# Kernel optimization log

Hardware: AMD Instinct MI355X
Metric: run time of the kernel (lower is better)

The kernel has to match this reference:

```python
import jax, jax.numpy as jnp
import numpy as np

TEMP = 0.07


def setup_inputs() -> dict:
    key = jax.random.key(0)
    k1, k2 = jax.random.split(key)
    N, C = 8192, 512
    X = jax.random.normal(k1, (N, C), dtype=jnp.float32)
    Y = jax.random.normal(k2, (N, C), dtype=jnp.float32)
    return {"X": X, "Y": Y}


def reference(X, Y):
    # Original loop computes, per row i, cross-entropy over logits
    # [X_i.Y_i, X_i.Y_j (j != i)] / temp with label 0 (the positive).
    # Softmax CE is permutation-invariant, so this equals
    #   logsumexp(S_i / temp) - S_ii / temp,  S = X @ Y^T,
    # summed over rows (loop accumulates with +=, i.e. sum reduction).
    S = jnp.einsum('nc,mc->nm', X, Y) / TEMP  # [N, N]
    lse = jax.nn.logsumexp(S, axis=1)          # [N]
    pos = jnp.diagonal(S)                      # [N]
    return jnp.sum(lse - pos)
```

## Files before the change

kernel.cpp:

```cpp
#include <hip/hip_runtime.h>
#include <stdint.h>

#define N 8192
#define C 512
#define BM 128
#define BN 128
#define BKF 128
#define NSPLIT 8
#define COLS_PER_SPLIT (N / NSPLIT)
#define CT (COLS_PER_SPLIT / BN)
#define GRID_GEMM (64 * NSPLIT)
#define INV_T 14.285714285714286f

typedef __attribute__((ext_vector_type(4)))  int   i32x4;
typedef __attribute__((ext_vector_type(8)))  int   i32x8;
typedef __attribute__((ext_vector_type(16))) float f32x16;

__global__ __launch_bounds__(256) void prep_kernel(const float* __restrict__ X,
                                                   const float* __restrict__ Y,
                                                   unsigned char* __restrict__ Xf8,
                                                   unsigned char* __restrict__ Yf8,
                                                   float* __restrict__ pos) {
  const int wave = threadIdx.x >> 6;
  const int lane = threadIdx.x & 63;
  const int row = blockIdx.x * 4 + wave;
  const float4* xr = (const float4*)(X + (size_t)row * C) + lane * 2;
  const float4* yr = (const float4*)(Y + (size_t)row * C) + lane * 2;
  float4 x0 = xr[0], x1 = xr[1];
  float4 y0 = yr[0], y1 = yr[1];
  float s = x0.x * y0.x + x0.y * y0.y + x0.z * y0.z + x0.w * y0.w
          + x1.x * y1.x + x1.y * y1.y + x1.z * y1.z + x1.w * y1.w;
  int2 ox, oy;
  ox.x = __builtin_amdgcn_cvt_pk_fp8_f32(x0.x, x0.y, 0, false);
  ox.x = __builtin_amdgcn_cvt_pk_fp8_f32(x0.z, x0.w, ox.x, true);
  ox.y = __builtin_amdgcn_cvt_pk_fp8_f32(x1.x, x1.y, 0, false);
  ox.y = __builtin_amdgcn_cvt_pk_fp8_f32(x1.z, x1.w, ox.y, true);
  oy.x = __builtin_amdgcn_cvt_pk_fp8_f32(y0.x, y0.y, 0, false);
  oy.x = __builtin_amdgcn_cvt_pk_fp8_f32(y0.z, y0.w, oy.x, true);
  oy.y = __builtin_amdgcn_cvt_pk_fp8_f32(y1.x, y1.y, 0, false);
  oy.y = __builtin_amdgcn_cvt_pk_fp8_f32(y1.z, y1.w, oy.y, true);
  ((int2*)(Xf8 + (size_t)row * C))[lane] = ox;
  ((int2*)(Yf8 + (size_t)row * C))[lane] = oy;
#pragma unroll
  for (int off = 32; off >= 1; off >>= 1) s += __shfl_xor(s, off);
  if (lane == 0) pos[row] = s * INV_T;
}

__global__ __launch_bounds__(256, 2) void gemm_lse_kernel(const unsigned char* __restrict__ Xf8,
                                                          const unsigned char* __restrict__ Yf8,
                                                          float2* __restrict__ partials) {
  __shared__ unsigned char As[BM][C];
  __shared__ unsigned char Bs[BN][BKF];

  const int tid = threadIdx.x;
  const int bx = blockIdx.x;
  const int split = bx & (NSPLIT - 1);
  const int rb = bx >> 3;
  const int row0 = rb * BM;
  const int colbase = split * COLS_PER_SPLIT;

  const int w = tid >> 6;
  const int lane = tid & 63;
  const int lrow = lane & 31;
  const int h = lane >> 5;
  const int arow = w * 32 + lrow;
  const int swz = lrow & 7;

#pragma unroll
  for (int t = 0; t < 16; ++t) {
    const int s2 = t * 256 + tid;
    const int r = s2 >> 5;
    const int cir = s2 & 31;
    const int k0t = cir >> 3;
    const int p = cir & 7;
    const int jj = p ^ (r & 7);
    const unsigned char* ga = Xf8 + (size_t)(row0 + r) * C + k0t * BKF + jj * 16;
    uint32_t loff = (uint32_t)((t * 256 + (tid & ~63)) * 16);
    __builtin_amdgcn_global_load_lds(
        (const __attribute__((address_space(1))) uint32_t*)(uintptr_t)ga,
        (__attribute__((address_space(3))) uint32_t*)(uintptr_t)((char*)&As[0][0] + loff),
        16, 0, 0);
  }

  float m_s[16], l_s[16];
#pragma unroll
  for (int s = 0; s < 16; ++s) { m_s[s] = -INFINITY; l_s[s] = 0.0f; }

  const int r_base = tid >> 3;
  const int p = tid & 7;
  const int j = p ^ (r_base & 7);

  for (int ct = 0; ct < CT; ++ct) {
    const int col0 = colbase + ct * BN;
    f32x16 acc[4];
#pragma unroll
    for (int t = 0; t < 4; ++t)
#pragma unroll
      for (int e = 0; e < 16; ++e) acc[t][e] = 0.0f;

    for (int k0 = 0; k0 < C / BKF; ++k0) {
#pragma unroll
      for (int i = 0; i < 4; ++i) {
        const int r = i * 32 + r_base;
        const unsigned char* gb = Yf8 + (size_t)(col0 + r) * C + k0 * BKF + j * 16;
        uint32_t loff = (uint32_t)((i * 256 + (tid & ~63)) * 16);
        __builtin_amdgcn_global_load_lds(
            (const __attribute__((address_space(1))) uint32_t*)(uintptr_t)gb,
            (__attribute__((address_space(3))) uint32_t*)(uintptr_t)((char*)&Bs[0][0] + loff),
            16, 0, 0);
      }
      __syncthreads();
#pragma unroll
      for (int s = 0; s < 2; ++s) {
        const int c0 = 4 * s + 2 * h;
        i32x4 alo = *(const i32x4*)&As[arow][k0 * BKF + (((c0    ) ^ swz) * 16)];
        i32x4 ahi = *(const i32x4*)&As[arow][k0 * BKF + (((c0 + 1) ^ swz) * 16)];
        i32x8 af = { alo[0], alo[1], alo[2], alo[3], ahi[0], ahi[1], ahi[2], ahi[3] };
#pragma unroll
        for (int tj = 0; tj < 4; ++tj) {
          const int brow = tj * 32 + lrow;
          i32x4 blo = *(const i32x4*)&Bs[brow][((c0    ) ^ swz) * 16];
          i32x4 bhi = *(const i32x4*)&Bs[brow][((c0 + 1) ^ swz) * 16];
          i32x8 bf = { blo[0], blo[1], blo[2], blo[3], bhi[0], bhi[1], bhi[2], bhi[3] };
          acc[tj] = __builtin_amdgcn_mfma_scale_f32_32x32x64_f8f6f4(
              af, bf, acc[tj], 0, 0, 0, 127, 0, 127);
        }
      }
      __syncthreads();
    }

#pragma unroll
    for (int r = 0; r < 16; ++r) {
      float v0 = acc[0][r] * INV_T;
      float v1 = acc[1][r] * INV_T;
      float v2 = acc[2][r] * INV_T;
      float v3 = acc[3][r] * INV_T;
      float mx = fmaxf(fmaxf(v0, v1), fmaxf(v2, v3));
      float mn = fmaxf(m_s[r], mx);
      l_s[r] = l_s[r] * __expf(m_s[r] - mn)
             + __expf(v0 - mn) + __expf(v1 - mn) + __expf(v2 - mn) + __expf(v3 - mn);
      m_s[r] = mn;
    }
  }

#pragma unroll
  for (int r = 0; r < 16; ++r) {
    float m = m_s[r], l = l_s[r];
#pragma unroll
    for (int off = 1; off < 32; off <<= 1) {
      float mo = __shfl_xor(m, off);
      float lo = __shfl_xor(l, off);
      float mn = fmaxf(m, mo);
      l = l * __expf(m - mn) + lo * __expf(mo - mn);
      m = mn;
    }
    m_s[r] = m; l_s[r] = l;
  }
  if (lrow == 0) {
#pragma unroll
    for (int r = 0; r < 16; ++r) {
      int row_local = (r & 3) + 8 * (r >> 2) + 4 * h;
      partials[(size_t)split * N + (row0 + w * 32 + row_local)] =
          make_float2(m_s[r], l_s[r]);
    }
  }
}

__global__ __launch_bounds__(256) void combine_kernel(const float2* __restrict__ partials,
                                                      const float* __restrict__ pos,
                                                      float* __restrict__ out) {
  int row = blockIdx.x * 256 + threadIdx.x;
  float M = -INFINITY, L = 0.0f;
#pragma unroll
  for (int s = 0; s < NSPLIT; ++s) {
    float2 pr = partials[(size_t)s * N + row];
    float mn = fmaxf(M, pr.x);
    L = L * __expf(M - mn) + pr.y * __expf(pr.x - mn);
    M = mn;
  }
  float v = M + __logf(L) - pos[row];
#pragma unroll
  for (int off = 32; off >= 1; off >>= 1) v += __shfl_xor(v, off);
  __shared__ float wsum[4];
  if ((threadIdx.x & 63) == 0) wsum[threadIdx.x >> 6] = v;
  __syncthreads();
  if (threadIdx.x == 0) atomicAdd(out, wsum[0] + wsum[1] + wsum[2] + wsum[3]);
}

extern "C" void kernel_launch(void* const* d_in, const int* in_sizes, int n_in,
                              void* d_out, int out_size, void* d_ws, size_t ws_size,
                              hipStream_t stream) {
  const float* X = (const float*)d_in[0];
  const float* Y = (const float*)d_in[1];
  float* out = (float*)d_out;

  char* w = (char*)d_ws;
  unsigned char* Xf8 = (unsigned char*)w;
  unsigned char* Yf8 = Xf8 + (size_t)N * C;
  float2* partials = (float2*)(Yf8 + (size_t)N * C);
  float* pos = (float*)((char*)partials + (size_t)NSPLIT * N * sizeof(float2));

  hipMemsetAsync(d_out, 0, sizeof(float), stream);
  prep_kernel<<<N / 4, 256, 0, stream>>>(X, Y, Xf8, Yf8, pos);
  gemm_lse_kernel<<<GRID_GEMM, 256, 0, stream>>>(Xf8, Yf8, partials);
  combine_kernel<<<N / 256, 256, 0, stream>>>(partials, pos, out);
}
```

Measured before the change: 123.2 us.

## Keep A fragments in registers and stage full-K B tile in LDS

The X row-block operand is no longer staged in shared memory. Each lane loads its whole A fragment for all K steps into registers once, and shared memory now holds one full-depth 128x512 B tile per column tile, loaded in a single pass. This removes the A LDS reads and cuts the barriers per column tile from eight to two. The cost is extra VGPR pressure from 64 persistent A registers under the two-blocks-per-SM launch bound. There is also still no double-buffering, so the B loads do not overlap compute.

```diff
diff --git a/kernel.cpp b/kernel.cpp
--- a/kernel.cpp
+++ b/kernel.cpp
@@ -5,11 +5,11 @@
 #define C 512
 #define BM 128
 #define BN 128
-#define BKF 128
 #define NSPLIT 8
 #define COLS_PER_SPLIT (N / NSPLIT)
 #define CT (COLS_PER_SPLIT / BN)
 #define GRID_GEMM (64 * NSPLIT)
+#define KSTEPS (C / 64)
 #define INV_T 14.285714285714286f
 
 typedef __attribute__((ext_vector_type(4)))  int   i32x4;
@@ -49,8 +49,7 @@
 __global__ __launch_bounds__(256, 2) void gemm_lse_kernel(const unsigned char* __restrict__ Xf8,
                                                           const unsigned char* __restrict__ Yf8,
                                                           float2* __restrict__ partials) {
-  __shared__ unsigned char As[BM][C];
-  __shared__ unsigned char Bs[BN][BKF];
+  __shared__ unsigned char Bs[BN][C];
 
   const int tid = threadIdx.x;
   const int bx = blockIdx.x;
@@ -66,29 +65,18 @@
   const int arow = w * 32 + lrow;
   const int swz = lrow & 7;
 
+  i32x8 a_frag[KSTEPS];
 #pragma unroll
-  for (int t = 0; t < 16; ++t) {
-    const int s2 = t * 256 + tid;
-    const int r = s2 >> 5;
-    const int cir = s2 & 31;
-    const int k0t = cir >> 3;
-    const int p = cir & 7;
-    const int jj = p ^ (r & 7);
-    const unsigned char* ga = Xf8 + (size_t)(row0 + r) * C + k0t * BKF + jj * 16;
-    uint32_t loff = (uint32_t)((t * 256 + (tid & ~63)) * 16);
-    __builtin_amdgcn_global_load_lds(
-        (const __attribute__((address_space(1))) uint32_t*)(uintptr_t)ga,
-        (__attribute__((address_space(3))) uint32_t*)(uintptr_t)((char*)&As[0][0] + loff),
-        16, 0, 0);
+  for (int s = 0; s < KSTEPS; ++s) {
+    const unsigned char* ga = Xf8 + (size_t)(row0 + arow) * C + s * 64 + h * 32;
+    i32x4 lo = *(const i32x4*)ga;
+    i32x4 hi = *(const i32x4*)(ga + 16);
+    a_frag[s] = i32x8{ lo[0], lo[1], lo[2], lo[3], hi[0], hi[1], hi[2], hi[3] };
   }
 
   float m_s[16], l_s[16];
 #pragma unroll
   for (int s = 0; s < 16; ++s) { m_s[s] = -INFINITY; l_s[s] = 0.0f; }
-
-  const int r_base = tid >> 3;
-  const int p = tid & 7;
-  const int j = p ^ (r_base & 7);
 
   for (int ct = 0; ct < CT; ++ct) {
     const int col0 = colbase + ct * BN;
@@ -98,35 +86,36 @@
 #pragma unroll
       for (int e = 0; e < 16; ++e) acc[t][e] = 0.0f;
 
-    for (int k0 = 0; k0 < C / BKF; ++k0) {
 #pragma unroll
-      for (int i = 0; i < 4; ++i) {
-        const int r = i * 32 + r_base;
-        const unsigned char* gb = Yf8 + (size_t)(col0 + r) * C + k0 * BKF + j * 16;
-        uint32_t loff = (uint32_t)((i * 256 + (tid & ~63)) * 16);
-        __builtin_amdgcn_global_load_lds(
-            (const __attribute__((address_space(1))) uint32_t*)(uintptr_t)gb,
-            (__attribute__((address_space(3))) uint32_t*)(uintptr_t)((char*)&Bs[0][0] + loff),
-            16, 0, 0);
+    for (int t = 0; t < 16; ++t) {
+      const int s2 = t * 256 + tid;
+      const int r = s2 >> 5;
+      const int cir = s2 & 31;
+      const int k0t = cir >> 3;
+      const int p = cir & 7;
+      const int jj = p ^ (r & 7);
+      const unsigned char* gb = Yf8 + (size_t)(col0 + r) * C + k0t * 128 + jj * 16;
+      uint32_t loff = (uint32_t)((t * 256 + (tid & ~63)) * 16);
+      __builtin_amdgcn_global_load_lds(
+          (const __attribute__((address_space(1))) uint32_t*)(uintptr_t)gb,
+          (__attribute__((address_space(3))) uint32_t*)(uintptr_t)((char*)&Bs[0][0] + loff),
+          16, 0, 0);
+    }
+    __syncthreads();
+
+#pragma unroll
+    for (int s = 0; s < KSTEPS; ++s) {
+      const int seg = (s >> 1) * 128;
+      const int c0 = (s & 1) * 4 + 2 * h;
+#pragma unroll
+      for (int tj = 0; tj < 4; ++tj) {
+        const int brow = tj * 32 + lrow;
+        i32x4 blo = *(const i32x4*)&Bs[brow][seg + (((c0    ) ^ swz) * 16)];
+        i32x4 bhi = *(const i32x4*)&Bs[brow][seg + (((c0 + 1) ^ swz) * 16)];
+        i32x8 bf = { blo[0], blo[1], blo[2], blo[3], bhi[0], bhi[1], bhi[2], bhi[3] };
+        acc[tj] = __builtin_amdgcn_mfma_scale_f32_32x32x64_f8f6f4(
+            a_frag[s], bf, acc[tj], 0, 0, 0, 127, 0, 127);
       }
-      __syncthreads();
-#pragma unroll
-      for (int s = 0; s < 2; ++s) {
-        const int c0 = 4 * s + 2 * h;
-        i32x4 alo = *(const i32x4*)&As[arow][k0 * BKF + (((c0    ) ^ swz) * 16)];
-        i32x4 ahi = *(const i32x4*)&As[arow][k0 * BKF + (((c0 + 1) ^ swz) * 16)];
-        i32x8 af = { alo[0], alo[1], alo[2], alo[3], ahi[0], ahi[1], ahi[2], ahi[3] };
-#pragma unroll
-        for (int tj = 0; tj < 4; ++tj) {
-          const int brow = tj * 32 + lrow;
-          i32x4 blo = *(const i32x4*)&Bs[brow][((c0    ) ^ swz) * 16];
-          i32x4 bhi = *(const i32x4*)&Bs[brow][((c0 + 1) ^ swz) * 16];
-          i32x8 bf = { blo[0], blo[1], blo[2], blo[3], bhi[0], bhi[1], bhi[2], bhi[3] };
-          acc[tj] = __builtin_amdgcn_mfma_scale_f32_32x32x64_f8f6f4(
-              af, bf, acc[tj], 0, 0, 0, 127, 0, 127);
-        }
-      }
-      __syncthreads();
     }
 
 #pragma unroll
@@ -141,6 +130,7 @@
              + __expf(v0 - mn) + __expf(v1 - mn) + __expf(v2 - mn) + __expf(v3 - mn);
       m_s[r] = mn;
     }
+    __syncthreads();
   }
 
 #pragma unroll
```

Result: slower. 126.7 us (+2.8%).
